# Kernel optimization log

Hardware: AMD Instinct MI355X
Metric: run time of the kernel (lower is better)

The kernel has to match this reference:

```python
import jax, jax.numpy as jnp
import numpy as np

H = 2048          # hidden_size
L_CACHE = 3       # depthwise conv kernel size
BATCH, SEQ = 2, 4096


def setup_inputs() -> dict:
    key = jax.random.key(0)
    k1, k2, k3, k4 = jax.random.split(key, 4)
    hidden_states = jax.random.normal(k1, (BATCH, SEQ, H), dtype=jnp.float32)
    # torch nn.Linear weights: [out_features, in_features]
    W_in = jax.random.normal(k2, (3 * H, H), dtype=jnp.float32) * (1.0 / np.sqrt(H))
    W_out = jax.random.normal(k3, (H, H), dtype=jnp.float32) * (1.0 / np.sqrt(H))
    # torch depthwise Conv1d weight: [H, 1, L]
    W_conv = jax.random.normal(k4, (H, 1, L_CACHE), dtype=jnp.float32) * (1.0 / np.sqrt(L_CACHE))
    return {"hidden_states": hidden_states, "W_in": W_in, "W_conv": W_conv, "W_out": W_out}


def reference(hidden_states, W_in, W_conv, W_out):
    # in_proj: [B,S,H] @ [H,3H] -> [B,S,3H]
    BCx = jnp.einsum('bsh,oh->bso', hidden_states, W_in)
    Bg, Cg, x = jnp.split(BCx, 3, axis=-1)   # each [B,S,H]
    Bx = Bg * x                              # gate before conv
    # depthwise causal conv over sequence: operate in NCH layout
    Bx_nch = jnp.transpose(Bx, (0, 2, 1))    # [B,H,S]
    conv_out = jax.lax.conv_general_dilated(
        Bx_nch, W_conv,
        window_strides=(1,),
        padding=[(L_CACHE - 1, 0)],          # causal: left pad only
        dimension_numbers=('NCH', 'OIH', 'NCH'),
        feature_group_count=H,
    )                                        # [B,H,S]
    y = Cg * jnp.transpose(conv_out, (0, 2, 1))  # C gating, back to [B,S,H]
    return jnp.einsum('bsh,oh->bso', y, W_out)   # out_proj
```

## Files before the change

### kernel.cpp

```cpp
#include <hip/hip_runtime.h>
#include <hip/hip_fp16.h>


typedef _Float16 f16x8 __attribute__((ext_vector_type(8)));
typedef float    f32x4 __attribute__((ext_vector_type(4)));

#define GLD_LDS16(gsrc, sdst) \
  __builtin_amdgcn_global_load_lds((const __attribute__((address_space(1))) void*)(gsrc), \
                                   (__attribute__((address_space(3))) void*)(sdst), 16, 0, 0)

#define VMCNT4 asm volatile("s_waitcnt vmcnt(4)" ::: "memory")
#define VMCNT0 asm volatile("s_waitcnt vmcnt(0)" ::: "memory")
#define LGKM0  asm volatile("s_waitcnt lgkmcnt(0)" ::: "memory")
#define BAR    __builtin_amdgcn_s_barrier()
#define FENCE  asm volatile("" ::: "memory")

__global__ __launch_bounds__(256) void cvt_all(const float* __restrict__ X,
                                               const float* __restrict__ Wi,
                                               const float* __restrict__ Wo,
                                               _Float16* __restrict__ Xh,
                                               _Float16* __restrict__ Wih,
                                               _Float16* __restrict__ Woh) {
  int base = (blockIdx.x * 256 + threadIdx.x) * 8;
  const float* src;
  _Float16* dst;
  int off;
  if (base < 16777216)      { src = X;  dst = Xh;  off = base; }
  else if (base < 29360128) { src = Wi; dst = Wih; off = base - 16777216; }
  else                      { src = Wo; dst = Woh; off = base - 29360128; }
  const float4* p = reinterpret_cast<const float4*>(src + off);
  float4 a = p[0], b = p[1];
  f16x8 o;
  o[0] = (_Float16)a.x; o[1] = (_Float16)a.y; o[2] = (_Float16)a.z; o[3] = (_Float16)a.w;
  o[4] = (_Float16)b.x; o[5] = (_Float16)b.y; o[6] = (_Float16)b.z; o[7] = (_Float16)b.w;
  *reinterpret_cast<f16x8*>(dst + off) = o;
}

__global__ __launch_bounds__(256) void conv_gate(const _Float16* __restrict__ BCx,
                                                 const float* __restrict__ Wc,
                                                 _Float16* __restrict__ Y) {
  const int h0 = threadIdx.x * 8;
  const int r0 = blockIdx.x * 8;
  const int s0 = r0 & 4095;

  float w0[8], w1[8], w2[8];
#pragma unroll
  for (int j = 0; j < 8; ++j) {
    w0[j] = Wc[(h0 + j) * 3 + 0];
    w1[j] = Wc[(h0 + j) * 3 + 1];
    w2[j] = Wc[(h0 + j) * 3 + 2];
  }

  float bxm2[8] = {}, bxm1[8] = {};
  if (s0 != 0) {
    const _Float16* pm2 = BCx + (size_t)(r0 - 2) * 6144 + h0;
    const _Float16* pm1 = BCx + (size_t)(r0 - 1) * 6144 + h0;
    f16x8 bg2 = *reinterpret_cast<const f16x8*>(pm2);
    f16x8 xx2 = *reinterpret_cast<const f16x8*>(pm2 + 4096);
    f16x8 bg1 = *reinterpret_cast<const f16x8*>(pm1);
    f16x8 xx1 = *reinterpret_cast<const f16x8*>(pm1 + 4096);
#pragma unroll
    for (int j = 0; j < 8; ++j) {
      bxm2[j] = (float)bg2[j] * (float)xx2[j];
      bxm1[j] = (float)bg1[j] * (float)xx1[j];
    }
  }

  for (int i = 0; i < 8; ++i) {
    const _Float16* pr = BCx + (size_t)(r0 + i) * 6144 + h0;
    f16x8 bg = *reinterpret_cast<const f16x8*>(pr);
    f16x8 cg = *reinterpret_cast<const f16x8*>(pr + 2048);
    f16x8 xx = *reinterpret_cast<const f16x8*>(pr + 4096);
    f16x8 o;
#pragma unroll
    for (int j = 0; j < 8; ++j) {
      float bx   = (float)bg[j] * (float)xx[j];
      float conv = w0[j] * bxm2[j] + w1[j] * bxm1[j] + w2[j] * bx;
      o[j] = (_Float16)((float)cg[j] * conv);
      bxm2[j] = bxm1[j];
      bxm1[j] = bx;
    }
    *reinterpret_cast<f16x8*>(Y + (size_t)(r0 + i) * 2048 + h0) = o;
  }
}

__device__ __forceinline__ void ldA(f16x8 (&af)[4][2], const _Float16* p, int base, int ak0, int ak1) {
#pragma unroll
  for (int i = 0; i < 4; ++i) {
    af[i][0] = *(const f16x8*)(p + base + i * 1024 + ak0);
    af[i][1] = *(const f16x8*)(p + base + i * 1024 + ak1);
  }
}
__device__ __forceinline__ void ldB(f16x8 (&bf)[2][2], const _Float16* p, int base, int ak0, int ak1) {
#pragma unroll
  for (int j = 0; j < 2; ++j) {
    bf[j][0] = *(const f16x8*)(p + base + j * 1024 + ak0);
    bf[j][1] = *(const f16x8*)(p + base + j * 1024 + ak1);
  }
}
template <int QM, int QN>
__device__ __forceinline__ void mfmaQ(f32x4 (&acc)[8][4], const f16x8 (&af)[4][2], const f16x8 (&bf)[2][2]) {
  __builtin_amdgcn_s_setprio(1);
#pragma unroll
  for (int i = 0; i < 4; ++i)
#pragma unroll
    for (int j = 0; j < 2; ++j)
#pragma unroll
      for (int ks = 0; ks < 2; ++ks)
        acc[QM * 4 + i][QN * 2 + j] =
            __builtin_amdgcn_mfma_f32_16x16x32_f16(af[i][ks], bf[j][ks], acc[QM * 4 + i][QN * 2 + j], 0, 0, 0);
  __builtin_amdgcn_s_setprio(0);
}

template <typename CT>
__global__ __launch_bounds__(512, 2) void gemm8p(const _Float16* __restrict__ Ag,
                                                 const _Float16* __restrict__ Bg,
                                                 CT* __restrict__ Cg,
                                                 int N, int K, int nbn) {
  __shared__ __align__(16) char smem[131072];
  const int tid = threadIdx.x, lane = tid & 63, w = tid >> 6;
  const int wr = w >> 2, wc = w & 3;

  const int nwg = (int)gridDim.x, q8 = nwg >> 3;
  const int swz = ((int)blockIdx.x & 7) * q8 + ((int)blockIdx.x >> 3);
  const int bm = (swz / nbn) << 8, bn = (swz % nbn) << 8;

  _Float16* const A0 = (_Float16*)(smem);
  _Float16* const B0 = (_Float16*)(smem + 32768);
  _Float16* const A1 = (_Float16*)(smem + 65536);
  _Float16* const B1 = (_Float16*)(smem + 98304);

  const int rr = tid >> 3;
  const int sCol = ((tid & 7) ^ (rr & 7)) * 8;
  const _Float16* aSrc = Ag + (size_t)(bm + rr) * K + sCol;
  const _Float16* bSrc = Bg + (size_t)(bn + (rr >> 5) * 64 + (rr & 31)) * K + sCol;

  const int ak0 = ((lane >> 4) ^ (lane & 7)) * 8;
  const int ak1 = (((lane >> 4) + 4) ^ (lane & 7)) * 8;
  const int aRB = (wr * 128 + (lane & 15)) * 64;
  const int bRB = (wc * 32 + (lane & 15)) * 64;

  const int nt = K >> 6;

#define STG_A(NBO, kt, u) GLD_LDS16(aSrc + (size_t)(u) * 64 * K + (kt) * 64, \
                                    smem + (NBO) + (u) * 8192 + tid * 16)
#define STG_B(NBO, kt, u) GLD_LDS16(bSrc + (size_t)(((u) & 1) * 128 + ((u) >> 1) * 32) * K + (kt) * 64, \
                                    smem + (NBO) + 32768 + (u) * 8192 + tid * 16)

  f16x8 af[4][2], bf[2][2];
  f32x4 acc[8][4] = {};

  STG_A(0, 0, 0); STG_A(0, 0, 2);
  STG_B(0, 0, 0); STG_B(0, 0, 1);
  STG_B(0, 0, 2); STG_B(0, 0, 3);
  STG_A(0, 0, 1); STG_A(0, 0, 3);
  VMCNT4; BAR; FENCE;

#define TILE(AB, BB, NBO, t)                                       \
  {                                                                \
    const int tn = ((t) + 1 < nt) ? (t) + 1 : nt - 1;              \
                                                  \
    ldA(af, AB, aRB, ak0, ak1);                                    \
    ldB(bf, BB, bRB, ak0, ak1);                                    \
    STG_A(NBO, tn, 0); STG_A(NBO, tn, 2);                          \
    VMCNT4; BAR; FENCE;                                            \
    mfmaQ<0, 0>(acc, af, bf);                                      \
                                                  \
    ldB(bf, BB, bRB + 8192, ak0, ak1);                             \
    STG_B(NBO, tn, 0); STG_B(NBO, tn, 1);                          \
    VMCNT4; BAR; FENCE;                                            \
    mfmaQ<0, 1>(acc, af, bf);                                      \
                                                  \
    ldA(af, AB, aRB + 4096, ak0, ak1);                             \
    STG_B(NBO, tn, 2); STG_B(NBO, tn, 3);                          \
    BAR; FENCE;                                                    \
    mfmaQ<1, 1>(acc, af, bf);                                      \
                                \
    ldB(bf, BB, bRB, ak0, ak1);                                    \
    STG_A(NBO, tn, 1); STG_A(NBO, tn, 3);                          \
    VMCNT4; BAR; FENCE;                                            \
    mfmaQ<1, 0>(acc, af, bf);                                      \
  }

  for (int t = 0; t < nt; t += 2) {
    TILE(A0, B0, 65536, t);
    TILE(A1, B1, 0, t + 1);
  }
  LGKM0; VMCNT0;

  const int rb = bm + wr * 128 + ((lane >> 4) << 2);
  const int cb = bn + wc * 64 + (lane & 15);
#pragma unroll
  for (int mi = 0; mi < 8; ++mi)
#pragma unroll
    for (int nj = 0; nj < 4; ++nj) {
      f32x4 v = acc[mi][nj];
#pragma unroll
      for (int rg = 0; rg < 4; ++rg)
        Cg[(size_t)(rb + mi * 16 + rg) * N + cb + nj * 16] = (CT)v[rg];
    }
#undef TILE
#undef STG_A
#undef STG_B
}

extern "C" void kernel_launch(void* const* d_in, const int* in_sizes, int n_in,
                              void* d_out, int out_size, void* d_ws, size_t ws_size,
                              hipStream_t stream) {
  const float* X  = (const float*)d_in[0];
  const float* Wi = (const float*)d_in[1];
  const float* Wc = (const float*)d_in[2];
  const float* Wo = (const float*)d_in[3];
  float* out = (float*)d_out;

  char* ws = (char*)d_ws;
  _Float16* Xh   = (_Float16*)(ws);
  _Float16* Wih  = (_Float16*)(ws + 33554432);
  _Float16* Woh  = (_Float16*)(ws + 58720256);
  _Float16* BCxh = (_Float16*)(ws + 67108864);
  _Float16* Yh   = (_Float16*)(ws + 167772160);
  (void)ws_size; (void)in_sizes; (void)n_in; (void)out_size;

  cvt_all<<<dim3(16384), 256, 0, stream>>>(X, Wi, Wo, Xh, Wih, Woh);

  gemm8p<_Float16><<<dim3(768), 512, 0, stream>>>(Xh, Wih, BCxh, 6144, 2048, 24);

  conv_gate<<<dim3(1024), 256, 0, stream>>>(BCxh, Wc, Yh);

  gemm8p<float><<<dim3(256), 512, 0, stream>>>(Yh, Woh, out, 2048, 2048, 8);
}
```

Measured before the change: 296.4 us.

## Restructure GEMM to K=32 tiles with four-stage LDS ring buffer

Rewrites the GEMM main loop to use 32-wide K tiles in a four-slot LDS ring instead of 64-wide K tiles with double buffering. Loads are now issued two tiles ahead. Each tile does two half-MFMA phases with lgkmcnt waits and sched barriers, and one block barrier per tile. The LDS swizzle is changed to match. The aim is deeper prefetch and fewer barriers per MFMA, at the cost of half the MFMA work per K step and more loop iterations.

```diff
diff --git a/kernel.cpp b/kernel.cpp
--- a/kernel.cpp
+++ b/kernel.cpp
@@ -13,6 +13,7 @@
 #define VMCNT0 asm volatile("s_waitcnt vmcnt(0)" ::: "memory")
 #define LGKM0  asm volatile("s_waitcnt lgkmcnt(0)" ::: "memory")
 #define BAR    __builtin_amdgcn_s_barrier()
+#define SCHED0 __builtin_amdgcn_sched_barrier(0)
 #define FENCE  asm volatile("" ::: "memory")
 
 __global__ __launch_bounds__(256) void cvt_all(const float* __restrict__ X,
@@ -84,40 +85,37 @@
   }
 }
 
-__device__ __forceinline__ void ldA(f16x8 (&af)[4][2], const _Float16* p, int base, int ak0, int ak1) {
-#pragma unroll
-  for (int i = 0; i < 4; ++i) {
-    af[i][0] = *(const f16x8*)(p + base + i * 1024 + ak0);
-    af[i][1] = *(const f16x8*)(p + base + i * 1024 + ak1);
-  }
-}
-__device__ __forceinline__ void ldB(f16x8 (&bf)[2][2], const _Float16* p, int base, int ak0, int ak1) {
-#pragma unroll
-  for (int j = 0; j < 2; ++j) {
-    bf[j][0] = *(const f16x8*)(p + base + j * 1024 + ak0);
-    bf[j][1] = *(const f16x8*)(p + base + j * 1024 + ak1);
-  }
-}
-template <int QM, int QN>
-__device__ __forceinline__ void mfmaQ(f32x4 (&acc)[8][4], const f16x8 (&af)[4][2], const f16x8 (&bf)[2][2]) {
+__device__ __forceinline__ void ldA4(f16x8 (&a)[4], const _Float16* p) {
+#pragma unroll
+  for (int i = 0; i < 4; ++i) a[i] = *(const f16x8*)(p + i * 512);
+}
+__device__ __forceinline__ void ldB2(f16x8 (&b)[2], const _Float16* p) {
+#pragma unroll
+  for (int j = 0; j < 2; ++j) b[j] = *(const f16x8*)(p + j * 512);
+}
+template <int QM>
+__device__ __forceinline__ void mfmaHalf(f32x4 (&acc)[8][4], const f16x8 (&a)[4],
+                                         const f16x8 (&b0)[2], const f16x8 (&b1)[2]) {
   __builtin_amdgcn_s_setprio(1);
 #pragma unroll
   for (int i = 0; i < 4; ++i)
 #pragma unroll
     for (int j = 0; j < 2; ++j)
-#pragma unroll
-      for (int ks = 0; ks < 2; ++ks)
-        acc[QM * 4 + i][QN * 2 + j] =
-            __builtin_amdgcn_mfma_f32_16x16x32_f16(af[i][ks], bf[j][ks], acc[QM * 4 + i][QN * 2 + j], 0, 0, 0);
+      acc[QM * 4 + i][j] = __builtin_amdgcn_mfma_f32_16x16x32_f16(a[i], b0[j], acc[QM * 4 + i][j], 0, 0, 0);
+#pragma unroll
+  for (int i = 0; i < 4; ++i)
+#pragma unroll
+    for (int j = 0; j < 2; ++j)
+      acc[QM * 4 + i][2 + j] = __builtin_amdgcn_mfma_f32_16x16x32_f16(a[i], b1[j], acc[QM * 4 + i][2 + j], 0, 0, 0);
   __builtin_amdgcn_s_setprio(0);
 }
 
 template <typename CT>
-__global__ __launch_bounds__(512, 2) void gemm8p(const _Float16* __restrict__ Ag,
+__global__ __launch_bounds__(512, 2) void gemm32(const _Float16* __restrict__ Ag,
                                                  const _Float16* __restrict__ Bg,
                                                  CT* __restrict__ Cg,
                                                  int N, int K, int nbn) {
-  __shared__ __align__(16) char smem[131072];
+  __shared__ __align__(16) _Float16 smem[65536];
   const int tid = threadIdx.x, lane = tid & 63, w = tid >> 6;
   const int wr = w >> 2, wc = w & 3;
 
@@ -125,68 +123,56 @@
   const int swz = ((int)blockIdx.x & 7) * q8 + ((int)blockIdx.x >> 3);
   const int bm = (swz / nbn) << 8, bn = (swz % nbn) << 8;
 
-  _Float16* const A0 = (_Float16*)(smem);
-  _Float16* const B0 = (_Float16*)(smem + 32768);
-  _Float16* const A1 = (_Float16*)(smem + 65536);
-  _Float16* const B1 = (_Float16*)(smem + 98304);
-
-  const int rr = tid >> 3;
-  const int sCol = ((tid & 7) ^ (rr & 7)) * 8;
-  const _Float16* aSrc = Ag + (size_t)(bm + rr) * K + sCol;
-  const _Float16* bSrc = Bg + (size_t)(bn + (rr >> 5) * 64 + (rr & 31)) * K + sCol;
-
-  const int ak0 = ((lane >> 4) ^ (lane & 7)) * 8;
-  const int ak1 = (((lane >> 4) + 4) ^ (lane & 7)) * 8;
-  const int aRB = (wr * 128 + (lane & 15)) * 64;
-  const int bRB = (wc * 32 + (lane & 15)) * 64;
-
-  const int nt = K >> 6;
-
-#define STG_A(NBO, kt, u) GLD_LDS16(aSrc + (size_t)(u) * 64 * K + (kt) * 64, \
-                                    smem + (NBO) + (u) * 8192 + tid * 16)
-#define STG_B(NBO, kt, u) GLD_LDS16(bSrc + (size_t)(((u) & 1) * 128 + ((u) >> 1) * 32) * K + (kt) * 64, \
-                                    smem + (NBO) + 32768 + (u) * 8192 + tid * 16)
-
-  f16x8 af[4][2], bf[2][2];
+  const int sCol = ((tid & 3) ^ ((tid >> 3) & 3)) * 8;
+  const _Float16* aSrc = Ag + (size_t)(bm + (tid >> 2)) * K + sCol;
+  const _Float16* bSrc = Bg + (size_t)(bn + (tid >> 2)) * K + sCol;
+
+  const int akc = (((lane >> 4) ^ ((lane >> 1) & 3))) * 8;
+  const int aoff = (wr * 128 + (lane & 15)) * 32 + akc;
+  const int boff = (wc * 64 + (lane & 15)) * 32 + akc;
+
+  const int nt = K >> 5;
+
+#define STG_A(BUF, kt, u) GLD_LDS16(aSrc + (size_t)(u) * 128 * K + (kt) * 32, \
+                                    (char*)smem + (BUF) * 16384 + (u) * 8192 + tid * 16)
+#define STG_B(BUF, kt, u) GLD_LDS16(bSrc + (size_t)(u) * 128 * K + (kt) * 32, \
+                                    (char*)smem + 65536 + (BUF) * 16384 + (u) * 8192 + tid * 16)
+
+  f16x8 afL[4], afH[4];
+  f16x8 bfE0[2], bfE1[2], bfO0[2], bfO1[2];
   f32x4 acc[8][4] = {};
 
-  STG_A(0, 0, 0); STG_A(0, 0, 2);
-  STG_B(0, 0, 0); STG_B(0, 0, 1);
-  STG_B(0, 0, 2); STG_B(0, 0, 3);
-  STG_A(0, 0, 1); STG_A(0, 0, 3);
+  STG_A(0, 0, 0); STG_A(0, 0, 1); STG_B(0, 0, 0); STG_B(0, 0, 1);
+  STG_A(1, 1, 0); STG_A(1, 1, 1); STG_B(1, 1, 0); STG_B(1, 1, 1);
   VMCNT4; BAR; FENCE;
 
-#define TILE(AB, BB, NBO, t)                                       \
-  {                                                                \
-    const int tn = ((t) + 1 < nt) ? (t) + 1 : nt - 1;              \
-                                                  \
-    ldA(af, AB, aRB, ak0, ak1);                                    \
-    ldB(bf, BB, bRB, ak0, ak1);                                    \
-    STG_A(NBO, tn, 0); STG_A(NBO, tn, 2);                          \
-    VMCNT4; BAR; FENCE;                                            \
-    mfmaQ<0, 0>(acc, af, bf);                                      \
-                                                  \
-    ldB(bf, BB, bRB + 8192, ak0, ak1);                             \
-    STG_B(NBO, tn, 0); STG_B(NBO, tn, 1);                          \
-    VMCNT4; BAR; FENCE;                                            \
-    mfmaQ<0, 1>(acc, af, bf);                                      \
-                                                  \
-    ldA(af, AB, aRB + 4096, ak0, ak1);                             \
-    STG_B(NBO, tn, 2); STG_B(NBO, tn, 3);                          \
-    BAR; FENCE;                                                    \
-    mfmaQ<1, 1>(acc, af, bf);                                      \
-                                \
-    ldB(bf, BB, bRB, ak0, ak1);                                    \
-    STG_A(NBO, tn, 1); STG_A(NBO, tn, 3);                          \
-    VMCNT4; BAR; FENCE;                                            \
-    mfmaQ<1, 0>(acc, af, bf);                                      \
-  }
-
-  for (int t = 0; t < nt; t += 2) {
-    TILE(A0, B0, 65536, t);
-    TILE(A1, B1, 0, t + 1);
-  }
-  LGKM0; VMCNT0;
+#define TILE(RB, SB, t, BF0, BF1)                                    \
+  {                                                                  \
+    const int tn = ((t) + 2 < nt) ? (t) + 2 : nt - 1;                \
+    const _Float16* Ab = smem + (RB) * 8192;                         \
+    const _Float16* Bb = smem + 32768 + (RB) * 8192;                 \
+                                                            \
+    ldA4(afL, Ab + aoff);                                            \
+    ldB2(BF0, Bb + boff);                                            \
+    ldB2(BF1, Bb + boff + 1024);                                     \
+    STG_A(SB, tn, 0); STG_A(SB, tn, 1);                              \
+    LGKM0; SCHED0;                                                   \
+    mfmaHalf<0>(acc, afL, BF0, BF1);                                 \
+                                                            \
+    ldA4(afH, Ab + aoff + 2048);                                     \
+    STG_B(SB, tn, 0); STG_B(SB, tn, 1);                              \
+    LGKM0; SCHED0;                                                   \
+    mfmaHalf<1>(acc, afH, BF0, BF1);                                 \
+    VMCNT4; BAR; FENCE;                                              \
+  }
+
+  for (int t = 0; t < nt; t += 4) {
+    TILE(0, 2, t,     bfE0, bfE1);
+    TILE(1, 3, t + 1, bfO0, bfO1);
+    TILE(2, 0, t + 2, bfE0, bfE1);
+    TILE(3, 1, t + 3, bfO0, bfO1);
+  }
+  VMCNT0;
 
   const int rb = bm + wr * 128 + ((lane >> 4) << 2);
   const int cb = bn + wc * 64 + (lane & 15);
@@ -223,9 +209,9 @@
 
   cvt_all<<<dim3(16384), 256, 0, stream>>>(X, Wi, Wo, Xh, Wih, Woh);
 
-  gemm8p<_Float16><<<dim3(768), 512, 0, stream>>>(Xh, Wih, BCxh, 6144, 2048, 24);
+  gemm32<_Float16><<<dim3(768), 512, 0, stream>>>(Xh, Wih, BCxh, 6144, 2048, 24);
 
   conv_gate<<<dim3(1024), 256, 0, stream>>>(BCxh, Wc, Yh);
 
-  gemm8p<float><<<dim3(256), 512, 0, stream>>>(Yh, Woh, out, 2048, 2048, 8);
-}
+  gemm32<float><<<dim3(256), 512, 0, stream>>>(Yh, Woh, out, 2048, 2048, 8);
+}
```

After: 316.3 us. 1.07x slower.

## Interleave B and x weight rows to fuse B*x gating into in_proj epilogue

Applied to the files above, without the earlier changes.

The conversion kernel now permutes W_in rows so the B and x projections of each channel land in adjacent output columns. The in_proj GEMM epilogue then multiplies neighbouring lanes via a lane shuffle and writes Bx and Cg as separate fp16 arrays, so the x projection is never written out. This cuts the GEMM output traffic and the conv kernel's reads from three streams to two. In exchange it adds shuffles and strided half-width stores in the epilogue, where only even lanes write for the Bx half.

```diff
diff --git a/kernel.cpp b/kernel.cpp
--- a/kernel.cpp
+++ b/kernel.cpp
@@ -24,21 +24,29 @@
   int base = (blockIdx.x * 256 + threadIdx.x) * 8;
   const float* src;
   _Float16* dst;
-  int off;
-  if (base < 16777216)      { src = X;  dst = Xh;  off = base; }
-  else if (base < 29360128) { src = Wi; dst = Wih; off = base - 16777216; }
-  else                      { src = Wo; dst = Woh; off = base - 29360128; }
-  const float4* p = reinterpret_cast<const float4*>(src + off);
+  if (base < 16777216) {
+    src = X + base; dst = Xh + base;
+  } else if (base < 29360128) {
+    int off = base - 16777216;
+    int row = off >> 11, col = off & 2047;
+    int rd = (row < 2048) ? (row << 1) : (row < 4096 ? row + 2048 : (((row - 4096) << 1) | 1));
+    src = Wi + off; dst = Wih + rd * 2048 + col;
+  } else {
+    int off = base - 29360128;
+    src = Wo + off; dst = Woh + off;
+  }
+  const float4* p = reinterpret_cast<const float4*>(src);
   float4 a = p[0], b = p[1];
   f16x8 o;
   o[0] = (_Float16)a.x; o[1] = (_Float16)a.y; o[2] = (_Float16)a.z; o[3] = (_Float16)a.w;
   o[4] = (_Float16)b.x; o[5] = (_Float16)b.y; o[6] = (_Float16)b.z; o[7] = (_Float16)b.w;
-  *reinterpret_cast<f16x8*>(dst + off) = o;
-}
-
-__global__ __launch_bounds__(256) void conv_gate(const _Float16* __restrict__ BCx,
-                                                 const float* __restrict__ Wc,
-                                                 _Float16* __restrict__ Y) {
+  *reinterpret_cast<f16x8*>(dst) = o;
+}
+
+__global__ __launch_bounds__(256) void conv_gate2(const _Float16* __restrict__ Bx,
+                                                  const _Float16* __restrict__ Cgb,
+                                                  const float* __restrict__ Wc,
+                                                  _Float16* __restrict__ Y) {
   const int h0 = threadIdx.x * 8;
   const int r0 = blockIdx.x * 8;
   const int s0 = r0 & 4095;
@@ -53,30 +61,21 @@
 
   float bxm2[8] = {}, bxm1[8] = {};
   if (s0 != 0) {
-    const _Float16* pm2 = BCx + (size_t)(r0 - 2) * 6144 + h0;
-    const _Float16* pm1 = BCx + (size_t)(r0 - 1) * 6144 + h0;
-    f16x8 bg2 = *reinterpret_cast<const f16x8*>(pm2);
-    f16x8 xx2 = *reinterpret_cast<const f16x8*>(pm2 + 4096);
-    f16x8 bg1 = *reinterpret_cast<const f16x8*>(pm1);
-    f16x8 xx1 = *reinterpret_cast<const f16x8*>(pm1 + 4096);
+    f16x8 b2 = *reinterpret_cast<const f16x8*>(Bx + (size_t)(r0 - 2) * 2048 + h0);
+    f16x8 b1 = *reinterpret_cast<const f16x8*>(Bx + (size_t)(r0 - 1) * 2048 + h0);
+#pragma unroll
+    for (int j = 0; j < 8; ++j) { bxm2[j] = (float)b2[j]; bxm1[j] = (float)b1[j]; }
+  }
+
+  for (int i = 0; i < 8; ++i) {
+    f16x8 bxv = *reinterpret_cast<const f16x8*>(Bx  + (size_t)(r0 + i) * 2048 + h0);
+    f16x8 cgv = *reinterpret_cast<const f16x8*>(Cgb + (size_t)(r0 + i) * 2048 + h0);
+    f16x8 o;
 #pragma unroll
     for (int j = 0; j < 8; ++j) {
-      bxm2[j] = (float)bg2[j] * (float)xx2[j];
-      bxm1[j] = (float)bg1[j] * (float)xx1[j];
-    }
-  }
-
-  for (int i = 0; i < 8; ++i) {
-    const _Float16* pr = BCx + (size_t)(r0 + i) * 6144 + h0;
-    f16x8 bg = *reinterpret_cast<const f16x8*>(pr);
-    f16x8 cg = *reinterpret_cast<const f16x8*>(pr + 2048);
-    f16x8 xx = *reinterpret_cast<const f16x8*>(pr + 4096);
-    f16x8 o;
-#pragma unroll
-    for (int j = 0; j < 8; ++j) {
-      float bx   = (float)bg[j] * (float)xx[j];
+      float bx   = (float)bxv[j];
       float conv = w0[j] * bxm2[j] + w1[j] * bxm1[j] + w2[j] * bx;
-      o[j] = (_Float16)((float)cg[j] * conv);
+      o[j] = (_Float16)((float)cgv[j] * conv);
       bxm2[j] = bxm1[j];
       bxm1[j] = bx;
     }
@@ -112,10 +111,12 @@
   __builtin_amdgcn_s_setprio(0);
 }
 
-template <typename CT>
+template <typename CT, int MODE>
 __global__ __launch_bounds__(512, 2) void gemm8p(const _Float16* __restrict__ Ag,
                                                  const _Float16* __restrict__ Bg,
-                                                 CT* __restrict__ Cg,
+                                                 CT* __restrict__ Cg_out,
+                                                 _Float16* __restrict__ BxP,
+                                                 _Float16* __restrict__ CgP,
                                                  int N, int K, int nbn) {
   __shared__ __align__(16) char smem[131072];
   const int tid = threadIdx.x, lane = tid & 63, w = tid >> 6;
@@ -159,23 +160,19 @@
 #define TILE(AB, BB, NBO, t)                                       \
   {                                                                \
     const int tn = ((t) + 1 < nt) ? (t) + 1 : nt - 1;              \
-                                                  \
     ldA(af, AB, aRB, ak0, ak1);                                    \
     ldB(bf, BB, bRB, ak0, ak1);                                    \
     STG_A(NBO, tn, 0); STG_A(NBO, tn, 2);                          \
     VMCNT4; BAR; FENCE;                                            \
     mfmaQ<0, 0>(acc, af, bf);                                      \
-                                                  \
     ldB(bf, BB, bRB + 8192, ak0, ak1);                             \
     STG_B(NBO, tn, 0); STG_B(NBO, tn, 1);                          \
     VMCNT4; BAR; FENCE;                                            \
     mfmaQ<0, 1>(acc, af, bf);                                      \
-                                                  \
     ldA(af, AB, aRB + 4096, ak0, ak1);                             \
     STG_B(NBO, tn, 2); STG_B(NBO, tn, 3);                          \
     BAR; FENCE;                                                    \
     mfmaQ<1, 1>(acc, af, bf);                                      \
-                                \
     ldB(bf, BB, bRB, ak0, ak1);                                    \
     STG_A(NBO, tn, 1); STG_A(NBO, tn, 3);                          \
     VMCNT4; BAR; FENCE;                                            \
@@ -188,17 +185,46 @@
   }
   LGKM0; VMCNT0;
 
-  const int rb = bm + wr * 128 + ((lane >> 4) << 2);
-  const int cb = bn + wc * 64 + (lane & 15);
-#pragma unroll
-  for (int mi = 0; mi < 8; ++mi)
-#pragma unroll
-    for (int nj = 0; nj < 4; ++nj) {
-      f32x4 v = acc[mi][nj];
-#pragma unroll
-      for (int rg = 0; rg < 4; ++rg)
-        Cg[(size_t)(rb + mi * 16 + rg) * N + cb + nj * 16] = (CT)v[rg];
-    }
+  const int rb  = bm + wr * 128 + ((lane >> 4) << 2);
+  const int cbl = bn + wc * 64 + (lane & 15);
+  if (MODE == 0) {
+#pragma unroll
+    for (int mi = 0; mi < 8; ++mi)
+#pragma unroll
+      for (int nj = 0; nj < 4; ++nj) {
+        f32x4 v = acc[mi][nj];
+#pragma unroll
+        for (int rg = 0; rg < 4; ++rg)
+          Cg_out[(size_t)(rb + mi * 16 + rg) * N + cbl + nj * 16] = (CT)v[rg];
+      }
+  } else if (bn < 4096) {
+    const bool writer = ((lane & 1) == 0);
+#pragma unroll
+    for (int mi = 0; mi < 8; ++mi)
+#pragma unroll
+      for (int nj = 0; nj < 4; ++nj) {
+        f32x4 v = acc[mi][nj];
+        const int h = (cbl + nj * 16) >> 1;
+#pragma unroll
+        for (int rg = 0; rg < 4; ++rg) {
+          float part = __shfl_xor(v[rg], 1);
+          float p = v[rg] * part;
+          if (writer)
+            BxP[(size_t)(rb + mi * 16 + rg) * 2048 + h] = (_Float16)p;
+        }
+      }
+  } else {
+    const int hc = cbl - 4096;
+#pragma unroll
+    for (int mi = 0; mi < 8; ++mi)
+#pragma unroll
+      for (int nj = 0; nj < 4; ++nj) {
+        f32x4 v = acc[mi][nj];
+#pragma unroll
+        for (int rg = 0; rg < 4; ++rg)
+          CgP[(size_t)(rb + mi * 16 + rg) * 2048 + hc + nj * 16] = (_Float16)v[rg];
+      }
+  }
 #undef TILE
 #undef STG_A
 #undef STG_B
@@ -214,18 +240,19 @@
   float* out = (float*)d_out;
 
   char* ws = (char*)d_ws;
-  _Float16* Xh   = (_Float16*)(ws);
-  _Float16* Wih  = (_Float16*)(ws + 33554432);
-  _Float16* Woh  = (_Float16*)(ws + 58720256);
-  _Float16* BCxh = (_Float16*)(ws + 67108864);
-  _Float16* Yh   = (_Float16*)(ws + 167772160);
+  _Float16* Xh  = (_Float16*)(ws);
+  _Float16* Wih = (_Float16*)(ws + 33554432);
+  _Float16* Woh = (_Float16*)(ws + 58720256);
+  _Float16* Bx  = (_Float16*)(ws + 67108864);
+  _Float16* CgB = (_Float16*)(ws + 100663296);
+  _Float16* Yh  = (_Float16*)(ws + 134217728);
   (void)ws_size; (void)in_sizes; (void)n_in; (void)out_size;
 
   cvt_all<<<dim3(16384), 256, 0, stream>>>(X, Wi, Wo, Xh, Wih, Woh);
 
-  gemm8p<_Float16><<<dim3(768), 512, 0, stream>>>(Xh, Wih, BCxh, 6144, 2048, 24);
-
-  conv_gate<<<dim3(1024), 256, 0, stream>>>(BCxh, Wc, Yh);
-
-  gemm8p<float><<<dim3(256), 512, 0, stream>>>(Yh, Woh, out, 2048, 2048, 8);
-}
+  gemm8p<_Float16, 1><<<dim3(768), 512, 0, stream>>>(Xh, Wih, Bx, Bx, CgB, 6144, 2048, 24);
+
+  conv_gate2<<<dim3(1024), 256, 0, stream>>>(Bx, CgB, Wc, Yh);
+
+  gemm8p<float, 0><<<dim3(256), 512, 0, stream>>>(Yh, Woh, out, nullptr, nullptr, 2048, 2048, 8);
+}
```

Result: no change. 293.4 us (-1.0%).
